# Kernel optimization log

Measured on AMD Instinct MI355X. Metric: run time of the kernel, lower is better.

The kernel has to match this reference:

```python
import jax, jax.numpy as jnp
import numpy as np

V, D, NL, N, ED, K, DT = 32000, 256, 4, 16, 512, 4, 16  # dt_rank = ceil(256/16)
B, L = 2, 2048
EPS = 1e-5


def setup_inputs() -> dict:
    key = jax.random.key(0)
    ks = jax.random.split(key, 10)
    s = 0.02
    x = jax.random.randint(ks[0], (B, L), 0, V)
    embed_t = jax.random.normal(ks[1], (V, D)) * s
    rms_w = jnp.ones((NL, D))
    in_proj_w = jax.random.normal(ks[2], (NL, 2 * ED, D)) * s
    conv_w = jax.random.normal(ks[3], (NL, ED, K)) * 0.1
    conv_b = jnp.zeros((NL, ED))
    x_proj_w = jax.random.normal(ks[4], (NL, DT + 2 * N, ED)) * s
    dt_proj_w = jax.random.normal(ks[5], (NL, ED, DT)) * (DT ** -0.5)
    dt_proj_b = jax.random.uniform(ks[6], (NL, ED), minval=-4.0, maxval=-2.0)  # softplus -> small dt
    A_log = jnp.log(jnp.tile(jnp.arange(1, N + 1, dtype=jnp.float32), (NL, ED, 1)))  # S4D-real init
    D_p = jnp.ones((NL, ED))
    out_proj_w = jax.random.normal(ks[7], (NL, D, ED)) * s
    norm_w = jnp.ones(D)
    norm_b = jnp.zeros(D)
    head_w = jax.random.normal(ks[8], (V, D)) * s
    head_b = jnp.zeros(V)
    return dict(x=x, embed_t=embed_t, rms_w=rms_w, in_proj_w=in_proj_w, conv_w=conv_w,
                conv_b=conv_b, x_proj_w=x_proj_w, dt_proj_w=dt_proj_w, dt_proj_b=dt_proj_b,
                A_log=A_log, D_p=D_p, out_proj_w=out_proj_w, norm_w=norm_w, norm_b=norm_b,
                head_w=head_w, head_b=head_b)


def _rmsnorm(x, w):
    return x * jax.lax.rsqrt(jnp.mean(x * x, axis=-1, keepdims=True) + EPS) * w


def _layernorm(x, w, b):
    mu = jnp.mean(x, axis=-1, keepdims=True)
    var = jnp.mean((x - mu) ** 2, axis=-1, keepdims=True)
    return (x - mu) * jax.lax.rsqrt(var + EPS) * w + b


def _scan_combine(left, right):
    al, bl = left
    ar, br = right
    return (al * ar, ar * bl + br)


def _mamba_block(h, rw, ipw, cw, cb, xpw, dpw, dpb, alog, dp, opw):
    # h: (B, L, D). Residual block: h + mixer(rmsnorm(h))
    xin = _rmsnorm(h, rw)
    xz = xin @ ipw.T                      # (B, L, 2*ED)
    xc, z = jnp.split(xz, 2, axis=-1)
    # causal depthwise conv1d, kernel K, left-pad K-1 (== torch padding=K-1 then [:L])
    k = cw.shape[1]
    seqlen = xc.shape[1]
    xp = jnp.pad(xc, ((0, 0), (k - 1, 0), (0, 0)))
    xc = sum(xp[:, i:i + seqlen, :] * cw[:, i] for i in range(k)) + cb
    xc = jax.nn.silu(xc)
    # selective SSM
    dt_rank = dpw.shape[1]
    n = alog.shape[1]
    dbc = xc @ xpw.T                      # (B, L, dt_rank + 2N)
    delta, Bm, Cm = jnp.split(dbc, [dt_rank, dt_rank + n], axis=-1)
    delta = jax.nn.softplus(delta @ dpw.T + dpb)   # (B, L, ED)
    A = -jnp.exp(alog)                              # (ED, N)
    dA = jnp.exp(delta[..., None] * A)              # (B, L, ED, N)
    dBx = (delta[..., None] * Bm[:, :, None, :]) * xc[..., None]  # (B, L, ED, N)
    _, hs = jax.lax.associative_scan(_scan_combine, (dA, dBx), axis=1)  # h_t = dA_t*h_{t-1} + dBx_t
    y = jnp.einsum('blen,bln->ble', hs, Cm) + dp * xc
    y = y * jax.nn.silu(z)
    return h + y @ opw.T


def reference(x, embed_t, rms_w, in_proj_w, conv_w, conv_b, x_proj_w, dt_proj_w,
              dt_proj_b, A_log, D_p, out_proj_w, norm_w, norm_b, head_w, head_b):
    h = embed_t[x]                        # (B, L, D)
    for i in range(rms_w.shape[0]):
        h = _mamba_block(h, rms_w[i], in_proj_w[i], conv_w[i], conv_b[i], x_proj_w[i],
                         dt_proj_w[i], dt_proj_b[i], A_log[i], D_p[i], out_proj_w[i])
    hn = _layernorm(h, norm_w, norm_b)
    return hn @ head_w.T + head_b         # (B, L, V)
```

## Files before the change

kernel.cpp:

```cpp
#include <hip/hip_runtime.h>
#include <hip/hip_bf16.h>
#include <math.h>

#define Bq   2
#define Lq   2048
#define Dq   256
#define NLq  4
#define Nst  16
#define EDq  512
#define Kq   4
#define DTq  16
#define Vq   32000
#define Rq   (Bq*Lq)
#define NCv  64
#define LCv  (Lq/NCv)
#define RPB  4

typedef __attribute__((ext_vector_type(8))) __bf16 bf16x8v;
typedef __attribute__((ext_vector_type(4))) float f32x4v;
typedef __attribute__((address_space(1))) const void GV;
typedef __attribute__((address_space(3))) void LV;

__device__ __forceinline__ unsigned short to_bf16(float f) {
    unsigned int u = __float_as_uint(f);
    unsigned int r = (u + 0x7FFFu + ((u >> 16) & 1u)) >> 16;
    return (unsigned short)r;
}
__device__ __forceinline__ float from_bf16(unsigned short u) {
    return __uint_as_float(((unsigned int)u) << 16);
}

__global__ __launch_bounds__(256) void convert_all(const float* __restrict__ w_in,
                                                   const float* __restrict__ w_out,
                                                   const float* __restrict__ w_xp,
                                                   const float* __restrict__ w_head,
                                                   unsigned short* __restrict__ dst) {
    const int S1 = NLq * 1024 * Dq;
    const int S2 = S1 + NLq * Dq * EDq;
    const int S3 = S2 + NLq * 48 * EDq;
    int i = (blockIdx.x * 256 + threadIdx.x) * 4;
    const float* src;
    int off;
    if (i < S1)      { src = w_in;   off = i; }
    else if (i < S2) { src = w_out;  off = i - S1; }
    else if (i < S3) { src = w_xp;   off = i - S2; }
    else             { src = w_head; off = i - S3; }
    float4 v = *(const float4*)&src[off];
    ushort4 o;
    o.x = to_bf16(v.x); o.y = to_bf16(v.y); o.z = to_bf16(v.z); o.w = to_bf16(v.w);
    *(ushort4*)&dst[i] = o;
}

__global__ __launch_bounds__(256) void embed_kernel(const int* __restrict__ x,
                                                    const float* __restrict__ et,
                                                    float* __restrict__ h) {
    int r = blockIdx.x;
    int d = threadIdx.x;
    h[r * Dq + d] = et[x[r] * Dq + d];
}

__global__ __launch_bounds__(256) void rmsnorm_kernel(const float* __restrict__ h,
                                                      const float* __restrict__ w,
                                                      unsigned short* __restrict__ out) {
    int r = blockIdx.x;
    int d = threadIdx.x;
    float v = h[r * Dq + d];
    float ss = v * v;
#pragma unroll
    for (int o = 32; o > 0; o >>= 1) ss += __shfl_down(ss, o);
    __shared__ float sb[4];
    if ((threadIdx.x & 63) == 0) sb[threadIdx.x >> 6] = ss;
    __syncthreads();
    float tot = sb[0] + sb[1] + sb[2] + sb[3];
    float scale = rsqrtf(tot * (1.0f / Dq) + 1e-5f);
    out[r * Dq + d] = to_bf16(v * scale * w[d]);
}

__global__ __launch_bounds__(256) void layernorm_kernel(const float* __restrict__ h,
                                                        const float* __restrict__ w,
                                                        const float* __restrict__ b,
                                                        unsigned short* __restrict__ out) {
    int r = blockIdx.x;
    int d = threadIdx.x;
    float v = h[r * Dq + d];
    float s = v, s2 = v * v;
#pragma unroll
    for (int o = 32; o > 0; o >>= 1) { s += __shfl_down(s, o); s2 += __shfl_down(s2, o); }
    __shared__ float sb[8];
    if ((threadIdx.x & 63) == 0) { sb[threadIdx.x >> 6] = s; sb[4 + (threadIdx.x >> 6)] = s2; }
    __syncthreads();
    float S  = sb[0] + sb[1] + sb[2] + sb[3];
    float S2 = sb[4] + sb[5] + sb[6] + sb[7];
    float mu = S * (1.0f / Dq);
    float var = S2 * (1.0f / Dq) - mu * mu;
    out[r * Dq + d] = to_bf16((v - mu) * rsqrtf(var + 1e-5f) * w[d] + b[d]);
}

template<int BM, int BN, typename OT, bool ACC>
__global__ __launch_bounds__(256) void gemm_mfma(const unsigned short* __restrict__ A,
                                                 const unsigned short* __restrict__ W,
                                                 const float* __restrict__ bias,
                                                 OT* __restrict__ C,
                                                 int M, int N, int K) {
    constexpr int WGM = (BM == 128 && BN == 64) ? 4 : 2;
    constexpr int WGN = 4 / WGM;
    constexpr int MR = BM / (WGM * 16);
    constexpr int NR = BN / (WGN * 16);
    constexpr int AR = BM / 64;
    constexpr int BR = BN / 64;
    __shared__ unsigned short As[BM * 32];
    __shared__ unsigned short Bs[BN * 32];

    const int gx = gridDim.x;
    const int nwg = gx * gridDim.y;
    int flat = blockIdx.y * gx + blockIdx.x;
    if ((nwg & 7) == 0) {
        int cpx = nwg >> 3;
        flat = (flat & 7) * cpx + (flat >> 3);
    }
    const int m0 = (flat / gx) * BM, n0 = (flat % gx) * BN;

    const int tid = threadIdx.x;
    const int wid = tid >> 6, lane = tid & 63;
    const int wrow = (wid / WGN) * (BM / WGM);
    const int wcol = (wid % WGN) * (BN / WGN);

    f32x4v acc[MR][NR];
#pragma unroll
    for (int i = 0; i < MR; i++)
#pragma unroll
        for (int j = 0; j < NR; j++) acc[i][j] = (f32x4v){0.f, 0.f, 0.f, 0.f};

    const int srow = lane >> 2;
    const int skoff = (lane & 3) * 8;
    const unsigned short* gA = A + (size_t)(m0 + wid * (16 * AR) + srow) * K + skoff;
    unsigned short* lA = As + wid * (512 * AR) + lane * 8;
    const unsigned short* gW = W + (size_t)(n0 + wid * (16 * BR) + srow) * K + skoff;
    unsigned short* lB = Bs + wid * (512 * BR) + lane * 8;

    const int l15 = lane & 15, lk = (lane >> 4) * 8;

    for (int kt = 0; kt < K; kt += 32) {
        __syncthreads();
#pragma unroll
        for (int p = 0; p < AR; p++)
            __builtin_amdgcn_global_load_lds((GV*)(gA + kt + (size_t)p * 16 * K),
                                             (LV*)(lA + p * 512), 16, 0, 0);
#pragma unroll
        for (int p = 0; p < BR; p++)
            __builtin_amdgcn_global_load_lds((GV*)(gW + kt + (size_t)p * 16 * K),
                                             (LV*)(lB + p * 512), 16, 0, 0);
        __syncthreads();

        bf16x8v a[MR], b[NR];
#pragma unroll
        for (int i = 0; i < MR; i++)
            a[i] = *(const bf16x8v*)&As[(wrow + i * 16 + l15) * 32 + lk];
#pragma unroll
        for (int j = 0; j < NR; j++)
            b[j] = *(const bf16x8v*)&Bs[(wcol + j * 16 + l15) * 32 + lk];
#pragma unroll
        for (int i = 0; i < MR; i++)
#pragma unroll
            for (int j = 0; j < NR; j++)
                acc[i][j] = __builtin_amdgcn_mfma_f32_16x16x32_bf16(a[i], b[j], acc[i][j], 0, 0, 0);
    }

    const int rbase = m0 + wrow + (lane >> 4) * 4;
    const int cbase = n0 + wcol + l15;
#pragma unroll
    for (int i = 0; i < MR; i++) {
#pragma unroll
        for (int j = 0; j < NR; j++) {
            int col = cbase + j * 16;
            float bv = bias ? bias[col] : 0.f;
#pragma unroll
            for (int r = 0; r < 4; r++) {
                int row = rbase + i * 16 + r;
                float v = acc[i][j][r] + bv;
                OT* dst = &C[(size_t)row * N + col];
                if constexpr (__is_same(OT, unsigned short)) {
                    if constexpr (ACC) *dst = to_bf16(v + from_bf16(*dst));
                    else               *dst = to_bf16(v);
                } else {
                    if constexpr (ACC) *dst = v + *dst;
                    else               *dst = v;
                }
            }
        }
    }
}

__global__ __launch_bounds__(256) void mid_fused(const unsigned short* __restrict__ xz,
                                                 const float* __restrict__ cw,
                                                 const float* __restrict__ cb,
                                                 const unsigned short* __restrict__ xpw16,
                                                 const float* __restrict__ dtw,
                                                 const float* __restrict__ dtb,
                                                 unsigned short* __restrict__ xc,
                                                 float* __restrict__ dbc,
                                                 unsigned short* __restrict__ dlt) {
    const int r0 = blockIdx.x * RPB;
    const int l0 = r0 & (Lq - 1);
    const int tid = threadIdx.x;
    __shared__ float xcs[RPB][EDq];
    __shared__ float dbs[RPB][16];

#pragma unroll
    for (int ch = 0; ch < 2; ch++) {
        const int e = tid + ch * 256;
        const float4 wv = *(const float4*)&cw[e * 4];
        const float bb = cb[e];
        float x0 = 0.f, x1 = 0.f, x2 = 0.f;
        if (l0 > 0) {
            x0 = from_bf16(xz[(size_t)(r0 - 3) * 1024 + e]);
            x1 = from_bf16(xz[(size_t)(r0 - 2) * 1024 + e]);
            x2 = from_bf16(xz[(size_t)(r0 - 1) * 1024 + e]);
        }
#pragma unroll
        for (int t = 0; t < RPB; t++) {
            float x3 = from_bf16(xz[(size_t)(r0 + t) * 1024 + e]);
            float a = bb;
            a = fmaf(x0, wv.x, a);
            a = fmaf(x1, wv.y, a);
            a = fmaf(x2, wv.z, a);
            a = fmaf(x3, wv.w, a);
            float s = a / (1.0f + __expf(-a));
            xcs[t][e] = s;
            xc[(size_t)(r0 + t) * EDq + e] = to_bf16(s);
            x0 = x1; x1 = x2; x2 = x3;
        }
    }
    __syncthreads();

    const int j = tid >> 2, sub = tid & 3;
    const unsigned short* wr = &xpw16[j * EDq + sub * 128];
#pragma unroll
    for (int t = 0; t < RPB; t++) {
        float part = 0.f;
        if (j < 48) {
            const float* xr = &xcs[t][sub * 128];
            for (int k = 0; k < 128; k += 4) {
                ushort4 wv = *(const ushort4*)&wr[k];
                float4 xv = *(const float4*)&xr[k];
                part = fmaf(from_bf16(wv.x), xv.x, part);
                part = fmaf(from_bf16(wv.y), xv.y, part);
                part = fmaf(from_bf16(wv.z), xv.z, part);
                part = fmaf(from_bf16(wv.w), xv.w, part);
            }
        }
        part += __shfl_xor(part, 1);
        part += __shfl_xor(part, 2);
        if (j < 48 && sub == 0) {
            dbc[(size_t)(r0 + t) * 48 + j] = part;
            if (j < 16) dbs[t][j] = part;
        }
    }
    __syncthreads();

#pragma unroll
    for (int ch = 0; ch < 2; ch++) {
        const int e = tid + ch * 256;
        float wrg[16];
#pragma unroll
        for (int g = 0; g < 4; g++) {
            float4 v = *(const float4*)&dtw[e * 16 + g * 4];
            wrg[g * 4] = v.x; wrg[g * 4 + 1] = v.y; wrg[g * 4 + 2] = v.z; wrg[g * 4 + 3] = v.w;
        }
        const float bb = dtb[e];
#pragma unroll
        for (int t = 0; t < RPB; t++) {
            float a = bb;
#pragma unroll
            for (int k = 0; k < 16; k++) a = fmaf(dbs[t][k], wrg[k], a);
            float sp = (a > 20.f) ? a : log1pf(__expf(a));
            dlt[(size_t)(r0 + t) * EDq + e] = to_bf16(sp);
        }
    }
}

__global__ __launch_bounds__(256) void scan_pass1(const unsigned short* __restrict__ dlt,
                                                  const unsigned short* __restrict__ xc,
                                                  const float* __restrict__ dbc,
                                                  const float* __restrict__ A_log,
                                                  float* __restrict__ cA,
                                                  float* __restrict__ cB) {
    int gid = blockIdx.x * 256 + threadIdx.x;
    int sub = gid & 3;
    int e = (gid >> 2) & (EDq - 1);
    int bc = gid >> 11;
    int rbase = bc * LCv;

    float Aa[4];
#pragma unroll
    for (int k = 0; k < 4; k++) Aa[k] = -__expf(A_log[e * 16 + sub * 4 + k]);
    float pA[4] = {1.f, 1.f, 1.f, 1.f};
    float hB[4] = {0.f, 0.f, 0.f, 0.f};

#pragma unroll 4
    for (int t = 0; t < LCv; t++) {
        int r = rbase + t;
        float d = from_bf16(dlt[(size_t)r * EDq + e]);
        float xv = from_bf16(xc[(size_t)r * EDq + e]);
        float dx = d * xv;
        float4 Bm = *(const float4*)&dbc[(size_t)r * 48 + 16 + sub * 4];
        float Bk[4] = {Bm.x, Bm.y, Bm.z, Bm.w};
#pragma unroll
        for (int k = 0; k < 4; k++) {
            float dA = __expf(d * Aa[k]);
            hB[k] = fmaf(dA, hB[k], dx * Bk[k]);
            pA[k] *= dA;
        }
    }
    size_t ob = ((size_t)bc * EDq + e) * 16 + sub * 4;
    *(float4*)&cA[ob] = make_float4(pA[0], pA[1], pA[2], pA[3]);
    *(float4*)&cB[ob] = make_float4(hB[0], hB[1], hB[2], hB[3]);
}

__global__ __launch_bounds__(256) void scan_pass2(const unsigned short* __restrict__ dlt,
                                                  const unsigned short* __restrict__ xc,
                                                  const float* __restrict__ dbc,
                                                  const float* __restrict__ A_log,
                                                  const float* __restrict__ cA,
                                                  const float* __restrict__ cB,
                                                  const float* __restrict__ Dp,
                                                  const unsigned short* __restrict__ xz,
                                                  unsigned short* __restrict__ y) {
    int gid = blockIdx.x * 256 + threadIdx.x;
    int sub = gid & 3;
    int e = (gid >> 2) & (EDq - 1);
    int bc = gid >> 11;
    int c  = bc & (NCv - 1);
    int b0 = bc - c;
    int rbase = bc * LCv;

    float Aa[4];
#pragma unroll
    for (int k = 0; k < 4; k++) Aa[k] = -__expf(A_log[e * 16 + sub * 4 + k]);

    float hh[4] = {0.f, 0.f, 0.f, 0.f};
    {
        size_t base = ((size_t)b0 * EDq + e) * 16 + sub * 4;
#pragma unroll 4
        for (int cc = 0; cc < c; cc++) {
            float4 a4 = *(const float4*)&cA[base];
            float4 b4 = *(const float4*)&cB[base];
            hh[0] = fmaf(a4.x, hh[0], b4.x);
            hh[1] = fmaf(a4.y, hh[1], b4.y);
            hh[2] = fmaf(a4.z, hh[2], b4.z);
            hh[3] = fmaf(a4.w, hh[3], b4.w);
            base += (size_t)EDq * 16;
        }
    }
    const float Dv = Dp[e];

#pragma unroll 4
    for (int t = 0; t < LCv; t++) {
        int r = rbase + t;
        float d = from_bf16(dlt[(size_t)r * EDq + e]);
        float xv = from_bf16(xc[(size_t)r * EDq + e]);
        float dx = d * xv;
        float4 Bm = *(const float4*)&dbc[(size_t)r * 48 + 16 + sub * 4];
        float4 Cm = *(const float4*)&dbc[(size_t)r * 48 + 32 + sub * 4];
        float Bk[4] = {Bm.x, Bm.y, Bm.z, Bm.w};
        float Ck[4] = {Cm.x, Cm.y, Cm.z, Cm.w};
        float cacc = 0.f;
#pragma unroll
        for (int k = 0; k < 4; k++) {
            float dA = __expf(d * Aa[k]);
            hh[k] = fmaf(dA, hh[k], dx * Bk[k]);
            cacc = fmaf(hh[k], Ck[k], cacc);
        }
        cacc += __shfl_xor(cacc, 1);
        cacc += __shfl_xor(cacc, 2);
        if (sub == 0) {
            float yv = fmaf(Dv, xv, cacc);
            float zv = from_bf16(xz[(size_t)r * 1024 + EDq + e]);
            float sz = zv / (1.0f + __expf(-zv));
            y[(size_t)r * EDq + e] = to_bf16(yv * sz);
        }
    }
}

extern "C" void kernel_launch(void* const* d_in, const int* in_sizes, int n_in,
                              void* d_out, int out_size, void* d_ws, size_t ws_size,
                              hipStream_t stream) {
    const int*   x         = (const int*)d_in[0];
    const float* embed_t   = (const float*)d_in[1];
    const float* rms_w     = (const float*)d_in[2];
    const float* in_proj_w = (const float*)d_in[3];
    const float* conv_w    = (const float*)d_in[4];
    const float* conv_b    = (const float*)d_in[5];
    const float* x_proj_w  = (const float*)d_in[6];
    const float* dt_proj_w = (const float*)d_in[7];
    const float* dt_proj_b = (const float*)d_in[8];
    const float* A_log     = (const float*)d_in[9];
    const float* D_p       = (const float*)d_in[10];
    const float* out_proj_w= (const float*)d_in[11];
    const float* norm_w    = (const float*)d_in[12];
    const float* norm_b    = (const float*)d_in[13];
    const float* head_w    = (const float*)d_in[14];
    const float* head_b    = (const float*)d_in[15];
    float* out = (float*)d_out;

    const size_t CSZ = (size_t)Bq * NCv * EDq * Nst;

    float* ws = (float*)d_ws;
    float* h    = ws;
    float* dbc  = h   + (size_t)Rq * Dq;
    float* cA   = dbc + (size_t)Rq * 48;
    float* cB   = cA  + CSZ;
    float* fend = cB  + CSZ;

    unsigned short* xz16  = (unsigned short*)fend;
    unsigned short* xc16  = xz16  + (size_t)Rq * 1024;
    unsigned short* dlt16 = xc16  + (size_t)Rq * EDq;
    unsigned short* xin16 = dlt16 + (size_t)Rq * EDq;
    unsigned short* yb16  = xin16 + (size_t)Rq * Dq;
    unsigned short* hn16  = yb16  + (size_t)Rq * EDq;
    unsigned short* w16i  = hn16  + (size_t)Rq * Dq;
    unsigned short* w16o  = w16i  + (size_t)NLq * 1024 * Dq;
    unsigned short* w16xp = w16o  + (size_t)NLq * Dq * EDq;
    unsigned short* w16h  = w16xp + (size_t)NLq * 48 * EDq;

    const int TOTW = NLq * 1024 * Dq + NLq * Dq * EDq + NLq * 48 * EDq + Vq * Dq;
    convert_all<<<TOTW / 1024, 256, 0, stream>>>(in_proj_w, out_proj_w, x_proj_w,
                                                 head_w, w16i);

    embed_kernel<<<Rq, 256, 0, stream>>>(x, embed_t, h);

    for (int i = 0; i < NLq; i++) {
        rmsnorm_kernel<<<Rq, 256, 0, stream>>>(h, rms_w + i * Dq, xin16);
        gemm_mfma<128, 128, unsigned short, false>
            <<<dim3(1024 / 128, Rq / 128), 256, 0, stream>>>(
            xin16, w16i + (size_t)i * 1024 * Dq, nullptr, xz16, Rq, 1024, Dq);
        mid_fused<<<Rq / RPB, 256, 0, stream>>>(
            xz16, conv_w + i * EDq * Kq, conv_b + i * EDq,
            w16xp + (size_t)i * 48 * EDq,
            dt_proj_w + (size_t)i * EDq * DTq, dt_proj_b + i * EDq,
            xc16, dbc, dlt16);
        scan_pass1<<<(Bq * NCv * EDq * 4) / 256, 256, 0, stream>>>(
            dlt16, xc16, dbc, A_log + i * EDq * Nst, cA, cB);
        scan_pass2<<<(Bq * NCv * EDq * 4) / 256, 256, 0, stream>>>(
            dlt16, xc16, dbc, A_log + i * EDq * Nst, cA, cB, D_p + i * EDq, xz16, yb16);
        gemm_mfma<64, 64, float, true><<<dim3(Dq / 64, Rq / 64), 256, 0, stream>>>(
            yb16, w16o + (size_t)i * Dq * EDq, nullptr, h, Rq, Dq, EDq);
    }

    layernorm_kernel<<<Rq, 256, 0, stream>>>(h, norm_w, norm_b, hn16);
    gemm_mfma<128, 128, float, false><<<dim3(Vq / 128, Rq / 128), 256, 0, stream>>>(
        hn16, w16h, head_b, out, Rq, Vq, Dq);
}
```

Measured before the change: 631.0 us.

## Precompute chunk carry-in states in a separate combine kernel for scan

Adds a scan_combine kernel that sequentially combines per-chunk (A,B) summaries into an exclusive prefix state per chunk, stored in a new cP buffer. scan_pass2 now loads its initial state directly instead of each thread re-walking all preceding chunks, removing quadratic redundant work and load imbalance across chunks. It adds one extra kernel launch per layer and a low-parallelism serial pass over 64 chunks.

```diff
diff --git a/kernel.cpp b/kernel.cpp
--- a/kernel.cpp
+++ b/kernel.cpp
@@ -317,12 +317,25 @@
     *(float4*)&cB[ob] = make_float4(hB[0], hB[1], hB[2], hB[3]);
 }
 
+__global__ __launch_bounds__(256) void scan_combine(const float* __restrict__ cA,
+                                                    const float* __restrict__ cB,
+                                                    float* __restrict__ cP) {
+    int idx = blockIdx.x * 256 + threadIdx.x;
+    int en = idx & 8191;
+    int b = idx >> 13;
+    float hc = 0.f;
+    for (int c = 0; c < NCv; c++) {
+        size_t base = ((size_t)(b * NCv + c) << 13) + en;
+        cP[base] = hc;
+        hc = fmaf(cA[base], hc, cB[base]);
+    }
+}
+
 __global__ __launch_bounds__(256) void scan_pass2(const unsigned short* __restrict__ dlt,
                                                   const unsigned short* __restrict__ xc,
                                                   const float* __restrict__ dbc,
                                                   const float* __restrict__ A_log,
-                                                  const float* __restrict__ cA,
-                                                  const float* __restrict__ cB,
+                                                  const float* __restrict__ cP,
                                                   const float* __restrict__ Dp,
                                                   const unsigned short* __restrict__ xz,
                                                   unsigned short* __restrict__ y) {
@@ -330,27 +343,16 @@
     int sub = gid & 3;
     int e = (gid >> 2) & (EDq - 1);
     int bc = gid >> 11;
-    int c  = bc & (NCv - 1);
-    int b0 = bc - c;
     int rbase = bc * LCv;
 
     float Aa[4];
 #pragma unroll
     for (int k = 0; k < 4; k++) Aa[k] = -__expf(A_log[e * 16 + sub * 4 + k]);
-
-    float hh[4] = {0.f, 0.f, 0.f, 0.f};
+    float hh[4];
+    size_t pb = ((size_t)bc * EDq + e) * 16 + sub * 4;
     {
-        size_t base = ((size_t)b0 * EDq + e) * 16 + sub * 4;
-#pragma unroll 4
-        for (int cc = 0; cc < c; cc++) {
-            float4 a4 = *(const float4*)&cA[base];
-            float4 b4 = *(const float4*)&cB[base];
-            hh[0] = fmaf(a4.x, hh[0], b4.x);
-            hh[1] = fmaf(a4.y, hh[1], b4.y);
-            hh[2] = fmaf(a4.z, hh[2], b4.z);
-            hh[3] = fmaf(a4.w, hh[3], b4.w);
-            base += (size_t)EDq * 16;
-        }
+        float4 v = *(const float4*)&cP[pb];
+        hh[0] = v.x; hh[1] = v.y; hh[2] = v.z; hh[3] = v.w;
     }
     const float Dv = Dp[e];
 
@@ -410,7 +412,8 @@
     float* dbc  = h   + (size_t)Rq * Dq;
     float* cA   = dbc + (size_t)Rq * 48;
     float* cB   = cA  + CSZ;
-    float* fend = cB  + CSZ;
+    float* cP   = cB  + CSZ;
+    float* fend = cP  + CSZ;
 
     unsigned short* xz16  = (unsigned short*)fend;
     unsigned short* xc16  = xz16  + (size_t)Rq * 1024;
@@ -441,8 +444,9 @@
             xc16, dbc, dlt16);
         scan_pass1<<<(Bq * NCv * EDq * 4) / 256, 256, 0, stream>>>(
             dlt16, xc16, dbc, A_log + i * EDq * Nst, cA, cB);
+        scan_combine<<<(Bq * EDq * Nst) / 256, 256, 0, stream>>>(cA, cB, cP);
         scan_pass2<<<(Bq * NCv * EDq * 4) / 256, 256, 0, stream>>>(
-            dlt16, xc16, dbc, A_log + i * EDq * Nst, cA, cB, D_p + i * EDq, xz16, yb16);
+            dlt16, xc16, dbc, A_log + i * EDq * Nst, cP, D_p + i * EDq, xz16, yb16);
         gemm_mfma<64, 64, float, true><<<dim3(Dq / 64, Rq / 64), 256, 0, stream>>>(
             yb16, w16o + (size_t)i * Dq * EDq, nullptr, h, Rq, Dq, EDq);
     }
```

After: 615.2 us. 1.03x faster.
